# Performance work log

Measured on AMD Instinct MI355X. Metric: run time of the kernel, lower is better.

## Reference

```python
import jax, jax.numpy as jnp
import numpy as np
import math

B, S, D, H, DFF, E, TOPK = 2, 2048, 768, 12, 3072, 8, 2
DH = D // H
EPS = 1e-5


def _ln(x, g, b):
    mu = jnp.mean(x, axis=-1, keepdims=True)
    var = jnp.mean(jnp.square(x - mu), axis=-1, keepdims=True)
    return (x - mu) * jax.lax.rsqrt(var + EPS) * g + b


def _router(x, rw, rb):
    # x: [B,S,D] -> probs [B,S,E], topk indices [B,S,K]
    logits = jnp.einsum('bsd,de->bse', x, rw) + rb
    probs = jax.nn.softmax(logits, axis=-1)
    topv, topi = jax.lax.top_k(probs, TOPK)
    return probs, topv, topi


def setup_inputs() -> dict:
    key = jax.random.key(0)
    ks = jax.random.split(key, 12)
    s = 0.02
    inp = {
        'x': jax.random.normal(ks[0], (B, S, D), dtype=jnp.float32),
        'wq': jax.random.normal(ks[1], (D, D), dtype=jnp.float32) * s,
        'bq': jnp.zeros((D,), jnp.float32),
        'wk': jax.random.normal(ks[2], (D, D), dtype=jnp.float32) * s,
        'bk': jnp.zeros((D,), jnp.float32),
        'wv': jax.random.normal(ks[3], (D, D), dtype=jnp.float32) * s,
        'bv': jnp.zeros((D,), jnp.float32),
        'wo': jax.random.normal(ks[4], (D, D), dtype=jnp.float32) * s,
        'bo': jnp.zeros((D,), jnp.float32),
        'norm1_g': jnp.ones((D,), jnp.float32),
        'norm1_b': jnp.zeros((D,), jnp.float32),
        'router_w': jax.random.normal(ks[5], (D, E), dtype=jnp.float32) * s,
        'router_b': jnp.zeros((E,), jnp.float32),
        'ew1': jax.random.normal(ks[6], (E, D, DFF), dtype=jnp.float32) * s,
        'eb1': jnp.zeros((E, DFF), jnp.float32),
        'ew2': jax.random.normal(ks[7], (E, DFF, D), dtype=jnp.float32) * s,
        'eb2': jnp.zeros((E, D), jnp.float32),
        'norm2_g': jnp.ones((D,), jnp.float32),
        'norm2_b': jnp.zeros((D,), jnp.float32),
    }
    return inp


def reference(x, wq, bq, wk, bk, wv, bv, wo, bo,
              norm1_g, norm1_b, router_w, router_b,
              ew1, eb1, ew2, eb2, norm2_g, norm2_b):
    # ---- multi-head self-attention ----
    def proj(w, b):
        return (jnp.einsum('bsd,de->bse', x, w) + b).reshape(B, S, H, DH).transpose(0, 2, 1, 3)
    q, k, v = proj(wq, bq), proj(wk, bk), proj(wv, bv)
    scores = jnp.einsum('bhqd,bhkd->bhqk', q, k) / math.sqrt(DH)
    attn = jax.nn.softmax(scores, axis=-1)
    ctx = jnp.einsum('bhqk,bhkd->bhqd', attn, v).transpose(0, 2, 1, 3).reshape(B, S, D)
    attn_out = jnp.einsum('bsd,de->bse', ctx, wo) + bo
    x1 = _ln(x + attn_out, norm1_g, norm1_b)

    # ---- MoE: top-k routing with renormalized gates ----
    probs, topv, topi = _router(x1, router_w, router_b)
    gates = topv / jnp.sum(topv, axis=-1, keepdims=True)          # [B,S,K]
    # combine weights per expert: [B,S,E]
    combine = jnp.sum(jax.nn.one_hot(topi, E, dtype=x1.dtype) * gates[..., None], axis=-2)
    moe_out = jnp.zeros_like(x1)
    for e in range(E):  # fixed small expert count
        h = jax.nn.relu(jnp.einsum('bsd,df->bsf', x1, ew1[e]) + eb1[e])
        y = jnp.einsum('bsf,fd->bsd', h, ew2[e]) + eb2[e]
        moe_out = moe_out + combine[..., e:e + 1] * y
    x2 = _ln(x1 + moe_out, norm2_g, norm2_b)

    # ---- redundant second router call + load-balancing aux loss ----
    probs2, _, topi2 = _router(x2, router_w, router_b)
    mask2 = jax.nn.one_hot(topi2, E, dtype=x2.dtype)              # [B,S,K,E]
    frac = jnp.mean(mask2, axis=(0, 1, 2))                        # fraction routed per expert
    prob = jnp.mean(probs2, axis=(0, 1))                          # mean router prob per expert
    aux_loss = E * jnp.sum(frac * prob)
    return (x2, aux_loss)
```

## Files before the change

### kernel.cpp

```cpp
#include <hip/hip_runtime.h>

typedef _Float16 f16;
typedef _Float16 f16x8 __attribute__((ext_vector_type(8)));
typedef _Float16 f16x4v __attribute__((ext_vector_type(4)));
typedef float f32x4 __attribute__((ext_vector_type(4)));

#define THREADS 256
#define BM 128
#define BN 128
#define BKK 64

#define WSCALE 256.0f
#define WDESCALE (1.0f/256.0f)

static __device__ __forceinline__ float wred_sum(float x){
#pragma unroll
  for (int o = 32; o; o >>= 1) x += __shfl_xor(x, o);
  return x;
}
static __device__ __forceinline__ int wred_sumi(int x){
#pragma unroll
  for (int o = 32; o; o >>= 1) x += __shfl_xor(x, o);
  return x;
}
static __device__ __forceinline__ float bred_sum(float x){
  __shared__ float r[4];
  x = wred_sum(x);
  if ((threadIdx.x & 63) == 0) r[threadIdx.x >> 6] = x;
  __syncthreads();
  float s = r[0] + r[1] + r[2] + r[3];
  __syncthreads();
  return s;
}

template<class Epi>
static __device__ __forceinline__ void gemm_core(const f16* A, const f16* BT,
                                                 int m0, int K, int N, int n0, Epi epi)
{
  __shared__ __align__(16) f16 Al[BM][BKK];
  __shared__ __align__(16) f16 Bl[BN][BKK];
  const int t = threadIdx.x;
  const int lane = t & 63, wave = t >> 6;
  const int wr = wave >> 1, wc = wave & 1;

  const f16* gA[4];
  const f16* gB[4];
#pragma unroll
  for (int i = 0; i < 4; ++i) {
    int c = i * THREADS + t;
    int r = c >> 3;
    int kc = (((c & 7) ^ (r & 7)) << 3);
    gA[i] = A + (size_t)(m0 + r) * K + kc;
    gB[i] = BT + (size_t)(n0 + r) * K + kc;
  }

  f32x4 acc[4][4];
#pragma unroll
  for (int i = 0; i < 4; ++i)
#pragma unroll
    for (int j = 0; j < 4; ++j)
#pragma unroll
      for (int r = 0; r < 4; ++r) acc[i][j][r] = 0.0f;

  f16* Als = &Al[0][0];
  f16* Bls = &Bl[0][0];

  for (int k0 = 0; k0 < K; k0 += BKK) {
    __syncthreads();
#pragma unroll
    for (int i = 0; i < 4; ++i) {
      int c = i * THREADS + t;
      __builtin_amdgcn_global_load_lds(
          (const __attribute__((address_space(1))) void*)(gA[i] + k0),
          (__attribute__((address_space(3))) void*)(Als + (size_t)c * 8), 16, 0, 0);
      __builtin_amdgcn_global_load_lds(
          (const __attribute__((address_space(1))) void*)(gB[i] + k0),
          (__attribute__((address_space(3))) void*)(Bls + (size_t)c * 8), 16, 0, 0);
    }
    __syncthreads();
#pragma unroll
    for (int kk = 0; kk < BKK; kk += 32) {
      const int lrow = lane & 15, lk = (lane >> 4) * 8;
      const int sx = (lrow & 7) << 3;
      f16x8 af[4], bf[4];
#pragma unroll
      for (int mf = 0; mf < 4; ++mf)
        af[mf] = *(const f16x8*)&Als[(size_t)(wr * 64 + mf * 16 + lrow) * BKK + ((kk + lk) ^ sx)];
#pragma unroll
      for (int nf = 0; nf < 4; ++nf)
        bf[nf] = *(const f16x8*)&Bls[(size_t)(wc * 64 + nf * 16 + lrow) * BKK + ((kk + lk) ^ sx)];
#pragma unroll
      for (int mf = 0; mf < 4; ++mf)
#pragma unroll
        for (int nf = 0; nf < 4; ++nf)
          acc[mf][nf] = __builtin_amdgcn_mfma_f32_16x16x32_f16(af[mf], bf[nf], acc[mf][nf], 0, 0, 0);
    }
  }
  const int lr4 = (lane >> 4) * 4, lc = lane & 15;
#pragma unroll
  for (int mf = 0; mf < 4; ++mf)
#pragma unroll
    for (int nf = 0; nf < 4; ++nf)
#pragma unroll
      for (int r = 0; r < 4; ++r) {
        int row = wr * 64 + mf * 16 + lr4 + r;
        int col = n0 + wc * 64 + nf * 16 + lc;
        epi(row, col, acc[mf][nf][r]);
      }
}

__global__ __launch_bounds__(256) void k_cvt(const float* x, f16* o){
  size_t i = (size_t)blockIdx.x * 256 + threadIdx.x;
  float4 v = ((const float4*)x)[i];
  f16x4v h;
  h[0] = (f16)v.x; h[1] = (f16)v.y; h[2] = (f16)v.z; h[3] = (f16)v.w;
  *(f16x4v*)(o + i * 4) = h;
}

__global__ __launch_bounds__(256) void k_transpose(const float* in, f16* out, int Kd, int Nd){
  __shared__ float tl[32][33];
  const float* ip = in + (size_t)blockIdx.z * Kd * Nd;
  f16* op = out + (size_t)blockIdx.z * Kd * Nd;
  int n0 = blockIdx.x * 32, k0 = blockIdx.y * 32;
  int tx = threadIdx.x & 31, ty = threadIdx.x >> 5;
#pragma unroll
  for (int j = 0; j < 32; j += 8) tl[ty + j][tx] = ip[(size_t)(k0 + ty + j) * Nd + n0 + tx];
  __syncthreads();
#pragma unroll
  for (int j = 0; j < 32; j += 8) op[(size_t)(n0 + ty + j) * Kd + k0 + tx] = (f16)(tl[tx][ty + j] * WSCALE);
}

__global__ __launch_bounds__(256) void k_gemm_qkv(const f16* xb,
    const f16* wqT, const f16* wkT, const f16* wvT,
    const float* bq, const float* bk, const float* bv,
    f16* Q, f16* Ko, f16* V)
{
  int m0 = blockIdx.x * 128, n0 = blockIdx.y * 128, z = blockIdx.z;
  const f16* BT = (z == 0) ? wqT : ((z == 1) ? wkT : wvT);
  const float* bias = (z == 0) ? bq : ((z == 1) ? bk : bv);
  auto epi = [&](int row, int col, float vv) {
    int grow = m0 + row;
    int b = grow >> 11, s = grow & 2047;
    int h = col >> 6, dh = col & 63;
    float val = vv * WDESCALE + bias[col];
    if (z == 2) V[(((size_t)b * 12 + h) * 64 + dh) * 2048 + s] = (f16)val;
    else ((z == 0) ? Q : Ko)[(((size_t)b * 12 + h) * 2048 + s) * 64 + dh] = (f16)val;
  };
  gemm_core(xb, BT, m0, 768, 768, n0, epi);
}

__global__ __launch_bounds__(256, 4) void k_fattn(const f16* Qf, const f16* Kf,
                                                  const f16* Vf, float* Opart, float* lpart)
{
  __shared__ __align__(16) f16 Kl[64][72];
  __shared__ __align__(16) f16 Vl[64][72];
  __shared__ __align__(16) f16 Pl[64][72];
  const int t = threadIdx.x, lane = t & 63, wid = t >> 6;
  const int lc = lane & 15, g = lane >> 4;
  const int q0 = blockIdx.x * 64, bh = blockIdx.y, sp = blockIdx.z;
  const f16* Qh = Qf + (size_t)bh * 2048 * 64;
  const f16* Kh = Kf + ((size_t)bh * 2048 + sp * 1024) * 64;
  const f16* Vh = Vf + (size_t)bh * 64 * 2048 + sp * 1024;

  const float C1 = 0.125f * 1.44269504f;
  const float C2 = 9.0f - 2.0f * 1.44269504f;

  f16x8 aq[2];
#pragma unroll
  for (int kk = 0; kk < 2; ++kk)
    aq[kk] = *(const f16x8*)(Qh + (size_t)(q0 + wid * 16 + lc) * 64 + kk * 32 + g * 8);

  f32x4 acco[4];
  float l_[4];
#pragma unroll
  for (int nf = 0; nf < 4; ++nf)
#pragma unroll
    for (int r = 0; r < 4; ++r) acco[nf][r] = 0.f;
#pragma unroll
  for (int r = 0; r < 4; ++r) l_[r] = 0.f;

  f16x8 sk[2], sv[2];
#pragma unroll
  for (int i = 0; i < 2; ++i) {
    int c = i * 256 + t;
    sk[i] = *(const f16x8*)(Kh + (size_t)(c >> 3) * 64 + (c & 7) * 8);
    sv[i] = *(const f16x8*)(Vh + (size_t)(c >> 3) * 2048 + (c & 7) * 8);
  }

  for (int j = 0; j < 16; ++j) {
    __syncthreads();
#pragma unroll
    for (int i = 0; i < 2; ++i) {
      int c = i * 256 + t;
      *(f16x8*)&Kl[c >> 3][(c & 7) * 8] = sk[i];
      *(f16x8*)&Vl[c >> 3][(c & 7) * 8] = sv[i];
    }
    __syncthreads();

    if (j < 15) {
      const int kv1 = (j + 1) * 64;
#pragma unroll
      for (int i = 0; i < 2; ++i) {
        int c = i * 256 + t;
        sk[i] = *(const f16x8*)(Kh + (size_t)(kv1 + (c >> 3)) * 64 + (c & 7) * 8);
        sv[i] = *(const f16x8*)(Vh + (size_t)(c >> 3) * 2048 + kv1 + (c & 7) * 8);
      }
    }

    f32x4 acc[4];
#pragma unroll
    for (int nf = 0; nf < 4; ++nf)
#pragma unroll
      for (int r = 0; r < 4; ++r) acc[nf][r] = 0.f;
#pragma unroll
    for (int kk = 0; kk < 2; ++kk) {
      f16x8 bk[4];
#pragma unroll
      for (int nf = 0; nf < 4; ++nf) bk[nf] = *(const f16x8*)&Kl[nf * 16 + lc][kk * 32 + g * 8];
#pragma unroll
      for (int nf = 0; nf < 4; ++nf)
        acc[nf] = __builtin_amdgcn_mfma_f32_16x16x32_f16(aq[kk], bk[nf], acc[nf], 0, 0, 0);
    }

    {
      const int prow = wid * 16 + g * 4;
#pragma unroll
      for (int r = 0; r < 4; ++r) {
        float ls = 0.f;
#pragma unroll
        for (int nf = 0; nf < 4; ++nf) {
          float p = exp2f(fmaf(acc[nf][r], C1, C2));
          Pl[prow + r][nf * 16 + lc] = (f16)p;
          ls += p;
        }
        l_[r] += ls;
      }
    }

#pragma unroll
    for (int kk = 0; kk < 2; ++kk) {
      f16x8 ap, bv[4];
      ap = *(const f16x8*)&Pl[wid * 16 + lc][kk * 32 + g * 8];
#pragma unroll
      for (int nf = 0; nf < 4; ++nf) bv[nf] = *(const f16x8*)&Vl[nf * 16 + lc][kk * 32 + g * 8];
#pragma unroll
      for (int nf = 0; nf < 4; ++nf)
        acco[nf] = __builtin_amdgcn_mfma_f32_16x16x32_f16(ap, bv[nf], acco[nf], 0, 0, 0);
    }
  }

  float* Op = Opart + ((size_t)(sp * 24 + bh) * 2048 + q0) * 64;
  float* lp = lpart + (size_t)(sp * 24 + bh) * 2048 + q0;
#pragma unroll
  for (int r = 0; r < 4; ++r) {
    float lr = l_[r];
#pragma unroll
    for (int o = 1; o < 16; o <<= 1) lr += __shfl_xor(lr, o);
    if (lc == 0) lp[wid * 16 + g * 4 + r] = lr;
#pragma unroll
    for (int nf = 0; nf < 4; ++nf)
      Op[(size_t)(wid * 16 + g * 4 + r) * 64 + nf * 16 + lc] = acco[nf][r];
  }
}

__global__ __launch_bounds__(256) void k_attcomb(const float* Opart, const float* lpart, f16* ctx){
  size_t base = ((size_t)blockIdx.x * 256 + threadIdx.x) * 4;
  size_t row = base >> 6; int dh = base & 63;
  int bh = (int)(row >> 11), qr = (int)(row & 2047);
  int b = bh / 12, h = bh - b * 12;
  const float4 o0 = *(const float4*)(Opart + base);
  const float4 o1 = *(const float4*)(Opart + base + (size_t)24 * 2048 * 64);
  float inv = 1.f / (lpart[row] + lpart[row + 24 * 2048]);
  f16x4v hv;
  hv[0] = (f16)((o0.x + o1.x) * inv);
  hv[1] = (f16)((o0.y + o1.y) * inv);
  hv[2] = (f16)((o0.z + o1.z) * inv);
  hv[3] = (f16)((o0.w + o1.w) * inv);
  *(f16x4v*)(ctx + ((size_t)b * 2048 + qr) * 768 + h * 64 + dh) = hv;
}

__global__ __launch_bounds__(256) void k_gemm_oproj(const f16* ctx, const f16* woT,
    const float* bo, const float* x, float* x1pre)
{
  int m0 = blockIdx.x * 128, n0 = blockIdx.y * 128;
  auto epi = [&](int row, int col, float vv) {
    size_t i = (size_t)(m0 + row) * 768 + col;
    x1pre[i] = x[i] + vv * WDESCALE + bo[col];
  };
  gemm_core(ctx, woT, m0, 768, 768, n0, epi);
}

__global__ __launch_bounds__(256) void k_ln(const float* in, const float* add,
    const float* g, const float* b, float* outf, f16* outh)
{
  size_t row = blockIdx.x;
  int t = threadIdx.x;
  const float* p = in + row * 768;
  float v[3];
  float s = 0.f;
#pragma unroll
  for (int i = 0; i < 3; ++i) {
    float xv = p[t + i * 256];
    if (add) xv += add[row * 768 + t + i * 256];
    v[i] = xv; s += xv;
  }
  float mu = bred_sum(s) * (1.f / 768.f);
  float q = 0.f;
#pragma unroll
  for (int i = 0; i < 3; ++i) { float d = v[i] - mu; q += d * d; }
  float var = bred_sum(q) * (1.f / 768.f);
  float inv = rsqrtf(var + 1e-5f);
#pragma unroll
  for (int i = 0; i < 3; ++i) {
    int c = t + i * 256;
    float y = (v[i] - mu) * inv * g[c] + b[c];
    outf[row * 768 + c] = y;
    if (outh) outh[row * 768 + c] = (f16)y;
  }
}

__global__ __launch_bounds__(256) void k_ln_moe(const float* x1, const f16* ys,
    const int* inv_map, const float* gates, const float* g, const float* b, float* outf)
{
  size_t row = blockIdx.x;
  int t = threadIdx.x;
  int sl0 = inv_map[row * 2], sl1 = inv_map[row * 2 + 1];
  float g0 = gates[row * 2], g1 = gates[row * 2 + 1];
  const float* p = x1 + row * 768;
  const f16* y0 = ys + (size_t)sl0 * 768;
  const f16* y1 = ys + (size_t)sl1 * 768;
  float v[3];
  float s = 0.f;
#pragma unroll
  for (int i = 0; i < 3; ++i) {
    int c = t + i * 256;
    float xv = p[c] + g0 * (float)y0[c] + g1 * (float)y1[c];
    v[i] = xv; s += xv;
  }
  float mu = bred_sum(s) * (1.f / 768.f);
  float q = 0.f;
#pragma unroll
  for (int i = 0; i < 3; ++i) { float d = v[i] - mu; q += d * d; }
  float var = bred_sum(q) * (1.f / 768.f);
  float inv = rsqrtf(var + 1e-5f);
#pragma unroll
  for (int i = 0; i < 3; ++i) {
    int c = t + i * 256;
    outf[row * 768 + c] = (v[i] - mu) * inv * g[c] + b[c];
  }
}

__global__ __launch_bounds__(256) void k_router(const float* X, const float* rw, const float* rb,
    int* topi, float* gates, float* pprob_part, int* pcnt_part, int mode)
{
  __shared__ float sp[4][8];
  __shared__ int   si[4][2];
  int wave = threadIdx.x >> 6;
  int tok = blockIdx.x * 4 + wave;
  int lane = threadIdx.x & 63;
  const float* xr = X + (size_t)tok * 768;
  float a0=0,a1=0,a2=0,a3=0,a4=0,a5=0,a6=0,a7=0;
#pragma unroll
  for (int i = 0; i < 12; ++i) {
    int d = lane + i * 64;
    float xv = xr[d];
    float4 w0 = *(const float4*)(rw + d * 8);
    float4 w1 = *(const float4*)(rw + d * 8 + 4);
    a0 += xv*w0.x; a1 += xv*w0.y; a2 += xv*w0.z; a3 += xv*w0.w;
    a4 += xv*w1.x; a5 += xv*w1.y; a6 += xv*w1.z; a7 += xv*w1.w;
  }
  a0=wred_sum(a0); a1=wred_sum(a1); a2=wred_sum(a2); a3=wred_sum(a3);
  a4=wred_sum(a4); a5=wred_sum(a5); a6=wred_sum(a6); a7=wred_sum(a7);
  if (lane == 0) {
    float lg[8] = {a0+rb[0],a1+rb[1],a2+rb[2],a3+rb[3],a4+rb[4],a5+rb[5],a6+rb[6],a7+rb[7]};
    float mx = lg[0];
    for (int e = 1; e < 8; ++e) mx = fmaxf(mx, lg[e]);
    float pp[8], ssum = 0.f;
    for (int e = 0; e < 8; ++e) { pp[e] = expf(lg[e] - mx); ssum += pp[e]; }
    float invs = 1.f / ssum;
    for (int e = 0; e < 8; ++e) pp[e] *= invs;
    int i1 = 0; float p1 = pp[0];
    for (int e = 1; e < 8; ++e) if (pp[e] > p1) { p1 = pp[e]; i1 = e; }
    int i2 = -1; float p2 = -1.f;
    for (int e = 0; e < 8; ++e) if (e != i1 && pp[e] > p2) { p2 = pp[e]; i2 = e; }
    if (mode == 1) {
      float gs = 1.f / (p1 + p2);
      topi[tok*2] = i1; topi[tok*2+1] = i2;
      gates[tok*2] = p1*gs; gates[tok*2+1] = p2*gs;
    } else {
      for (int e = 0; e < 8; ++e) sp[wave][e] = pp[e];
      si[wave][0] = i1; si[wave][1] = i2;
    }
  }
  if (mode == 2) {
    __syncthreads();
    int t = threadIdx.x;
    if (t < 8) {
      float s = sp[0][t] + sp[1][t] + sp[2][t] + sp[3][t];
      int c = 0;
#pragma unroll
      for (int w = 0; w < 4; ++w) c += (si[w][0] == t) + (si[w][1] == t);
      pprob_part[blockIdx.x * 8 + t] = s;
      pcnt_part[blockIdx.x * 8 + t] = c;
    }
  }
}

__global__ __launch_bounds__(256) void k_plan(const int* topi, int* offal,
    int* tile_e, int* tile_r0, int* tile_e2, int* tile_r02)
{
  __shared__ int hist[8];
  int t = threadIdx.x, lane = t & 63;
  if (t < 8) hist[t] = 0;
  __syncthreads();
  int loc[8] = {0,0,0,0,0,0,0,0};
  for (int i = t; i < 8192; i += 256) ++loc[topi[i]];
#pragma unroll
  for (int e = 0; e < 8; ++e) {
    int s = wred_sumi(loc[e]);
    if (lane == 0) atomicAdd(&hist[e], s);
  }
  __syncthreads();
  if (t == 0) {
    int off = 0, t1 = 0, t2 = 0;
    for (int e = 0; e < 8; ++e) {
      offal[e] = off;
      int nt = (hist[e] + 255) >> 8;
      for (int i = 0; i < nt; ++i) {
        tile_e[t1] = e; tile_r0[t1] = off + i * 256; ++t1;
        tile_e2[t2] = e; tile_r02[t2] = off + i * 256; ++t2;
        tile_e2[t2] = e; tile_r02[t2] = off + i * 256 + 128; ++t2;
      }
      off += nt << 8;
    }
    for (; t1 < 40; ++t1) { tile_e[t1] = -1; tile_r0[t1] = 0; }
    for (; t2 < 80; ++t2) { tile_e2[t2] = -1; tile_r02[t2] = 0; }
  }
}

__global__ __launch_bounds__(512) void k_scatter(const int* topi, const float* gates,
    const int* offal, int* perm, float* gate_s, int* inv_map)
{
  int w = threadIdx.x >> 6, lane = threadIdx.x & 63;
  int base = offal[w];
  for (int it = 0; it < 128; ++it) {
    int i = it * 64 + lane;
    int e = topi[i];
    bool act = (e == w);
    unsigned long long mask = __ballot(act);
    if (act) {
      int pos = base + __popcll(mask & ((1ull << lane) - 1ull));
      perm[pos] = i >> 1;
      gate_s[pos] = gates[i];
      inv_map[i] = pos;
    }
    base += __popcll(mask);
  }
}

__global__ __launch_bounds__(256) void k_gather(const f16* x1b, const int* perm, f16* xg){
  size_t i = (size_t)blockIdx.x * 256 + threadIdx.x;
  int row = (int)(i / 96), col8 = (int)(i % 96);
  int src = perm[row];
  *(f16x8*)(xg + (size_t)row * 768 + col8 * 8) =
      *(const f16x8*)(x1b + (size_t)src * 768 + col8 * 8);
}

__global__ __launch_bounds__(512, 2) void k_gemm_moe1(const f16* xg, const f16* ew1T,
    const float* eb1, const int* tile_e, const int* tile_r0, f16* hbuf)
{
  __shared__ __align__(16) f16 Al[2][256][64];
  __shared__ __align__(16) f16 Bl[2][256][64];
  int e = tile_e[blockIdx.x];
  if (e < 0) return;
  int s0 = tile_r0[blockIdx.x];
  int n0 = blockIdx.y * 256;
  const f16* A  = xg + (size_t)s0 * 768;
  const f16* BT = ew1T + (size_t)e * 3072 * 768 + (size_t)n0 * 768;
  const float* be = eb1 + e * 3072;

  const int t = threadIdx.x;
  const int lane = t & 63, wave = t >> 6;
  const int wr = wave >> 2, wc = wave & 3;

  const f16* gA[4];
  const f16* gB[4];
#pragma unroll
  for (int i = 0; i < 4; ++i) {
    int c = i * 512 + t;
    int r = c >> 3;
    int kc = (((c & 7) ^ (r & 7)) << 3);
    gA[i] = A + (size_t)r * 768 + kc;
    gB[i] = BT + (size_t)r * 768 + kc;
  }

  f32x4 acc[8][4];
#pragma unroll
  for (int i = 0; i < 8; ++i)
#pragma unroll
    for (int j = 0; j < 4; ++j)
#pragma unroll
      for (int r = 0; r < 4; ++r) acc[i][j][r] = 0.0f;

  auto stage = [&](int buf, int k0) {
    f16* Ad = &Al[buf][0][0];
    f16* Bd = &Bl[buf][0][0];
#pragma unroll
    for (int i = 0; i < 4; ++i) {
      int c = i * 512 + t;
      __builtin_amdgcn_global_load_lds(
          (const __attribute__((address_space(1))) void*)(gA[i] + k0),
          (__attribute__((address_space(3))) void*)(Ad + (size_t)c * 8), 16, 0, 0);
      __builtin_amdgcn_global_load_lds(
          (const __attribute__((address_space(1))) void*)(gB[i] + k0),
          (__attribute__((address_space(3))) void*)(Bd + (size_t)c * 8), 16, 0, 0);
    }
  };

  stage(0, 0);
  __syncthreads();

  int cur = 0;
  for (int ks = 0; ks < 12; ++ks) {
    if (ks < 11) stage(cur ^ 1, (ks + 1) * 64);
    const f16* Ab = &Al[cur][0][0];
    const f16* Bb = &Bl[cur][0][0];
#pragma unroll
    for (int kk = 0; kk < 64; kk += 32) {
      const int lrow = lane & 15, lk = (lane >> 4) * 8;
      const int sx = (lrow & 7) << 3;
      f16x8 af[8], bf[4];
#pragma unroll
      for (int mf = 0; mf < 8; ++mf)
        af[mf] = *(const f16x8*)&Ab[(size_t)(wr * 128 + mf * 16 + lrow) * 64 + ((kk + lk) ^ sx)];
#pragma unroll
      for (int nf = 0; nf < 4; ++nf)
        bf[nf] = *(const f16x8*)&Bb[(size_t)(wc * 64 + nf * 16 + lrow) * 64 + ((kk + lk) ^ sx)];
#pragma unroll
      for (int mf = 0; mf < 8; ++mf)
#pragma unroll
        for (int nf = 0; nf < 4; ++nf)
          acc[mf][nf] = __builtin_amdgcn_mfma_f32_16x16x32_f16(af[mf], bf[nf], acc[mf][nf], 0, 0, 0);
    }
    __syncthreads();
    cur ^= 1;
  }

  const int lr4 = (lane >> 4) * 4, lc = lane & 15;
#pragma unroll
  for (int mf = 0; mf < 8; ++mf)
#pragma unroll
    for (int nf = 0; nf < 4; ++nf)
#pragma unroll
      for (int r = 0; r < 4; ++r) {
        int row = wr * 128 + mf * 16 + lr4 + r;
        int col = n0 + wc * 64 + nf * 16 + lc;
        hbuf[(size_t)(s0 + row) * 3072 + col] = (f16)fmaxf(acc[mf][nf][r] * WDESCALE + be[col], 0.f);
      }
}

__global__ __launch_bounds__(256) void k_gemm_moe2(const f16* hbuf, const f16* ew2T,
    const float* eb2, const int* tile_e2, const int* tile_r02, f16* yslots)
{
  int e = tile_e2[blockIdx.x];
  if (e < 0) return;
  int s0 = tile_r02[blockIdx.x];
  int n0 = blockIdx.y * 128;
  const f16* A = hbuf + (size_t)s0 * 3072;
  const f16* BT = ew2T + (size_t)e * 768 * 3072;
  const float* be = eb2 + e * 768;
  auto epi = [&](int row, int col, float vv) {
    yslots[(size_t)(s0 + row) * 768 + col] = (f16)(vv * WDESCALE + be[col]);
  };
  gemm_core(A, BT, 0, 3072, 768, n0, epi);
}

__global__ __launch_bounds__(256) void k_final(const float* pprob, const int* pcnt, float* out){
  __shared__ float sp[256];
  __shared__ int sc[256];
  int t = threadIdx.x, e = t & 7, g = t >> 3;
  float s = 0.f; int c = 0;
  for (int b = g; b < 1024; b += 32) { s += pprob[b * 8 + e]; c += pcnt[b * 8 + e]; }
  sp[t] = s; sc[t] = c;
  __syncthreads();
  if (t < 8) {
    float ss = 0.f; int cc = 0;
    for (int g2 = 0; g2 < 32; ++g2) { ss += sp[t + g2 * 8]; cc += sc[t + g2 * 8]; }
    sp[t] = ss; sc[t] = cc;
  }
  __syncthreads();
  if (t == 0) {
    float a = 0.f;
    for (int e2 = 0; e2 < 8; ++e2)
      a += ((float)sc[e2] * (1.f / 8192.f)) * (sp[e2] * (1.f / 4096.f));
    out[(size_t)4096 * 768] = 8.f * a;
  }
}

extern "C" void kernel_launch(void* const* d_in, const int* in_sizes, int n_in,
                              void* d_out, int out_size, void* d_ws, size_t ws_size,
                              hipStream_t stream)
{
  const float* x   = (const float*)d_in[0];
  const float* wq  = (const float*)d_in[1];
  const float* bq  = (const float*)d_in[2];
  const float* wk  = (const float*)d_in[3];
  const float* bk  = (const float*)d_in[4];
  const float* wv  = (const float*)d_in[5];
  const float* bv  = (const float*)d_in[6];
  const float* wo  = (const float*)d_in[7];
  const float* bo  = (const float*)d_in[8];
  const float* n1g = (const float*)d_in[9];
  const float* n1b = (const float*)d_in[10];
  const float* rw  = (const float*)d_in[11];
  const float* rb  = (const float*)d_in[12];
  const float* ew1 = (const float*)d_in[13];
  const float* eb1 = (const float*)d_in[14];
  const float* ew2 = (const float*)d_in[15];
  const float* eb2 = (const float*)d_in[16];
  const float* n2g = (const float*)d_in[17];
  const float* n2b = (const float*)d_in[18];
  float* out = (float*)d_out;
  char* ws = (char*)d_ws;

  size_t oWQT,oWKT,oWVT,oWOT,oEW1T,oEW2T,oXB,oQ,oK,oV,oCTX,oX1,oX1B,oYS;
  size_t oTOPI,oGATES,oOFF,oTE,oTR,oTE2,oTR2,oPERM,oGS,oINV,oXG,oH,oPP,oPC,oOP,oLP;

  {
    size_t off = 0;
    auto al = [&](size_t bytes) { size_t o = off; off += (bytes + 255) & ~(size_t)255; return o; };
    oWQT = al((size_t)768*768*2); oWKT = al((size_t)768*768*2);
    oWVT = al((size_t)768*768*2); oWOT = al((size_t)768*768*2);
    oEW1T = al((size_t)8*768*3072*2); oEW2T = al((size_t)8*768*3072*2);
    oXB  = al((size_t)4096*768*2);
    oQ   = al((size_t)24*2048*64*2); oK = al((size_t)24*2048*64*2); oV = al((size_t)24*2048*64*2);
    oCTX = al((size_t)4096*768*2);
    oX1  = al((size_t)4096*768*4);
    oX1B = al((size_t)4096*768*2);
    oYS  = al((size_t)10240*768*2);
    oTOPI = al(4096*2*4); oGATES = al(4096*2*4);
    oOFF = al(256);
    oTE = al(256); oTR = al(256); oTE2 = al(512); oTR2 = al(512);
    oPERM = al(10240*4); oGS = al(10240*4); oINV = al(8192*4);
    oXG = al((size_t)10240*768*2);
    oH = al((size_t)10240*3072*2);
    oPP = al(1024*8*4); oPC = al(1024*8*4);
    oOP = al((size_t)2*24*2048*64*4);
    oLP = al((size_t)2*24*2048*4);
    (void)ws_size;
  }

  f16* wqT  = (f16*)(ws + oWQT);
  f16* wkT  = (f16*)(ws + oWKT);
  f16* wvT  = (f16*)(ws + oWVT);
  f16* woT  = (f16*)(ws + oWOT);
  f16* ew1T = (f16*)(ws + oEW1T);
  f16* ew2T = (f16*)(ws + oEW2T);
  f16* xb   = (f16*)(ws + oXB);
  f16* Qf   = (f16*)(ws + oQ);
  f16* Kf   = (f16*)(ws + oK);
  f16* Vf   = (f16*)(ws + oV);
  f16* ctxb = (f16*)(ws + oCTX);
  float* x1 = (float*)(ws + oX1);
  f16* x1bb = (f16*)(ws + oX1B);
  f16* yslots = (f16*)(ws + oYS);
  int* topi = (int*)(ws + oTOPI);
  float* gates = (float*)(ws + oGATES);
  int* offal  = (int*)(ws + oOFF);
  int* tile_e = (int*)(ws + oTE);
  int* tile_r0= (int*)(ws + oTR);
  int* tile_e2 = (int*)(ws + oTE2);
  int* tile_r02= (int*)(ws + oTR2);
  int* perm   = (int*)(ws + oPERM);
  float* gate_s = (float*)(ws + oGS);
  int* inv_map = (int*)(ws + oINV);
  f16* xg     = (f16*)(ws + oXG);
  f16* hbuf   = (f16*)(ws + oH);
  float* pprob = (float*)(ws + oPP);
  int* pcnt   = (int*)(ws + oPC);
  float* Opart = (float*)(ws + oOP);
  float* lpart = (float*)(ws + oLP);

  (void)in_sizes; (void)n_in; (void)out_size;

  hipMemsetAsync(ws + oPERM, 0, 2 * 10240 * 4, stream);

  k_cvt<<<3072, 256, 0, stream>>>(x, xb);
  k_transpose<<<dim3(24,24,1), 256, 0, stream>>>(wq, wqT, 768, 768);
  k_transpose<<<dim3(24,24,1), 256, 0, stream>>>(wk, wkT, 768, 768);
  k_transpose<<<dim3(24,24,1), 256, 0, stream>>>(wv, wvT, 768, 768);
  k_transpose<<<dim3(24,24,1), 256, 0, stream>>>(wo, woT, 768, 768);
  k_transpose<<<dim3(96,24,8), 256, 0, stream>>>(ew1, ew1T, 768, 3072);
  k_transpose<<<dim3(24,96,8), 256, 0, stream>>>(ew2, ew2T, 3072, 768);

  k_gemm_qkv<<<dim3(32,6,3), 256, 0, stream>>>(xb, wqT, wkT, wvT, bq, bk, bv, Qf, Kf, Vf);
  k_fattn<<<dim3(32,24,2), 256, 0, stream>>>(Qf, Kf, Vf, Opart, lpart);
  k_attcomb<<<3072, 256, 0, stream>>>(Opart, lpart, ctxb);
  k_gemm_oproj<<<dim3(32,6), 256, 0, stream>>>(ctxb, woT, bo, x, x1);
  k_ln<<<4096, 256, 0, stream>>>(x1, nullptr, n1g, n1b, x1, x1bb);

  k_router<<<1024, 256, 0, stream>>>(x1, rw, rb, topi, gates, pprob, pcnt, 1);
  k_plan<<<1, 256, 0, stream>>>(topi, offal, tile_e, tile_r0, tile_e2, tile_r02);
  k_scatter<<<1, 512, 0, stream>>>(topi, gates, offal, perm, gate_s, inv_map);
  k_gather<<<3840, 256, 0, stream>>>(x1bb, perm, xg);
  k_gemm_moe1<<<dim3(40,12), 512, 0, stream>>>(xg, ew1T, eb1, tile_e, tile_r0, hbuf);
  k_gemm_moe2<<<dim3(80,6), 256, 0, stream>>>(hbuf, ew2T, eb2, tile_e2, tile_r02, yslots);

  k_ln_moe<<<4096, 256, 0, stream>>>(x1, yslots, inv_map, gates, n2g, n2b, out);
  k_router<<<1024, 256, 0, stream>>>(out, rw, rb, topi, gates, pprob, pcnt, 2);
  k_final<<<1, 256, 0, stream>>>(pprob, pcnt, out);
}
```

Baseline: 457.0 us.

## Fuse MoE row gather into first expert GEMM and deepen load pipeline

Removes the separate gather kernel and intermediate xg buffer by having the first MoE GEMM load A rows through the perm index directly from x1b. It also restructures the K loop to prefetch two stages ahead, using explicit vmcnt waits and raw barriers instead of __syncthreads, and changes launch bounds to one block per CU. This saves a kernel launch and a write and read of the gathered activations, but adds indirect addressing. The launch-bounds change may lower occupancy.

```diff
diff --git a/kernel.cpp b/kernel.cpp
--- a/kernel.cpp
+++ b/kernel.cpp
@@ -458,16 +458,8 @@
   }
 }
 
-__global__ __launch_bounds__(256) void k_gather(const f16* x1b, const int* perm, f16* xg){
-  size_t i = (size_t)blockIdx.x * 256 + threadIdx.x;
-  int row = (int)(i / 96), col8 = (int)(i % 96);
-  int src = perm[row];
-  *(f16x8*)(xg + (size_t)row * 768 + col8 * 8) =
-      *(const f16x8*)(x1b + (size_t)src * 768 + col8 * 8);
-}
-
-__global__ __launch_bounds__(512, 2) void k_gemm_moe1(const f16* xg, const f16* ew1T,
-    const float* eb1, const int* tile_e, const int* tile_r0, f16* hbuf)
+__global__ __launch_bounds__(512, 1) void k_gemm_moe1(const f16* x1b, const f16* ew1T,
+    const float* eb1, const int* tile_e, const int* tile_r0, const int* perm, f16* hbuf)
 {
   __shared__ __align__(16) f16 Al[2][256][64];
   __shared__ __align__(16) f16 Bl[2][256][64];
@@ -475,7 +467,6 @@
   if (e < 0) return;
   int s0 = tile_r0[blockIdx.x];
   int n0 = blockIdx.y * 256;
-  const f16* A  = xg + (size_t)s0 * 768;
   const f16* BT = ew1T + (size_t)e * 3072 * 768 + (size_t)n0 * 768;
   const float* be = eb1 + e * 3072;
 
@@ -490,7 +481,7 @@
     int c = i * 512 + t;
     int r = c >> 3;
     int kc = (((c & 7) ^ (r & 7)) << 3);
-    gA[i] = A + (size_t)r * 768 + kc;
+    gA[i] = x1b + (size_t)perm[s0 + r] * 768 + kc;
     gB[i] = BT + (size_t)r * 768 + kc;
   }
 
@@ -518,11 +509,15 @@
   };
 
   stage(0, 0);
-  __syncthreads();
-
-  int cur = 0;
+  stage(1, 64);
+
   for (int ks = 0; ks < 12; ++ks) {
-    if (ks < 11) stage(cur ^ 1, (ks + 1) * 64);
+    const int cur = ks & 1;
+    if (ks < 11) asm volatile("s_waitcnt vmcnt(8)" ::: "memory");
+    else         asm volatile("s_waitcnt vmcnt(0)" ::: "memory");
+    __builtin_amdgcn_s_barrier();
+    asm volatile("" ::: "memory");
+
     const f16* Ab = &Al[cur][0][0];
     const f16* Bb = &Bl[cur][0][0];
 #pragma unroll
@@ -542,8 +537,11 @@
         for (int nf = 0; nf < 4; ++nf)
           acc[mf][nf] = __builtin_amdgcn_mfma_f32_16x16x32_f16(af[mf], bf[nf], acc[mf][nf], 0, 0, 0);
     }
-    __syncthreads();
-    cur ^= 1;
+
+    asm volatile("" ::: "memory");
+    __builtin_amdgcn_s_barrier();
+    asm volatile("" ::: "memory");
+    if (ks < 10) stage(cur, (ks + 2) * 64);
   }
 
   const int lr4 = (lane >> 4) * 4, lc = lane & 15;
@@ -624,7 +622,7 @@
   char* ws = (char*)d_ws;
 
   size_t oWQT,oWKT,oWVT,oWOT,oEW1T,oEW2T,oXB,oQ,oK,oV,oCTX,oX1,oX1B,oYS;
-  size_t oTOPI,oGATES,oOFF,oTE,oTR,oTE2,oTR2,oPERM,oGS,oINV,oXG,oH,oPP,oPC,oOP,oLP;
+  size_t oTOPI,oGATES,oOFF,oTE,oTR,oTE2,oTR2,oPERM,oGS,oINV,oH,oPP,oPC,oOP,oLP;
 
   {
     size_t off = 0;
@@ -642,7 +640,6 @@
     oOFF = al(256);
     oTE = al(256); oTR = al(256); oTE2 = al(512); oTR2 = al(512);
     oPERM = al(10240*4); oGS = al(10240*4); oINV = al(8192*4);
-    oXG = al((size_t)10240*768*2);
     oH = al((size_t)10240*3072*2);
     oPP = al(1024*8*4); oPC = al(1024*8*4);
     oOP = al((size_t)2*24*2048*64*4);
@@ -674,7 +671,6 @@
   int* perm   = (int*)(ws + oPERM);
   float* gate_s = (float*)(ws + oGS);
   int* inv_map = (int*)(ws + oINV);
-  f16* xg     = (f16*)(ws + oXG);
   f16* hbuf   = (f16*)(ws + oH);
   float* pprob = (float*)(ws + oPP);
   int* pcnt   = (int*)(ws + oPC);
@@ -702,8 +698,7 @@
   k_router<<<1024, 256, 0, stream>>>(x1, rw, rb, topi, gates, pprob, pcnt, 1);
   k_plan<<<1, 256, 0, stream>>>(topi, offal, tile_e, tile_r0, tile_e2, tile_r02);
   k_scatter<<<1, 512, 0, stream>>>(topi, gates, offal, perm, gate_s, inv_map);
-  k_gather<<<3840, 256, 0, stream>>>(x1bb, perm, xg);
-  k_gemm_moe1<<<dim3(40,12), 512, 0, stream>>>(xg, ew1T, eb1, tile_e, tile_r0, hbuf);
+  k_gemm_moe1<<<dim3(40,12), 512, 0, stream>>>(x1bb, ew1T, eb1, tile_e, tile_r0, perm, hbuf);
   k_gemm_moe2<<<dim3(80,6), 256, 0, stream>>>(hbuf, ew2T, eb2, tile_e2, tile_r02, yslots);
 
   k_ln_moe<<<4096, 256, 0, stream>>>(x1, yslots, inv_map, gates, n2g, n2b, out);
```

New measurement: 438.3 us. 4.1% less time.
